# Optimization experiments

Hardware: AMD Instinct MI355X
Metric: run time of the kernel (lower is better)

Reference implementation:

```python
import jax, jax.numpy as jnp
import numpy as np

B, CIN, T, H, W = 1, 256, 64, 32, 32
A, G = 8, 8
SCALES = jnp.array([1., 2., 4., 8., 16., 32., 64., 128.], dtype=jnp.float32)
FEAT_STRIDE = 8.0
NMS_TOP_N = 100
NMS_THRESH = 0.7
MIN_SIZE = 4.0
POS_THR, NEG_THR = 0.7, 0.3
NEG_INF = -1e9


def _conv3d(x, w, b, strides):
    y = jax.lax.conv_general_dilated(
        x, w, window_strides=strides, padding=[(1, 1)] * 3,
        dimension_numbers=('NCDHW', 'OIDHW', 'NCDHW'))
    return y + b[None, :, None, None, None]


def _iou(a, b):
    # 1D interval IoU; a, b broadcastable [..., 2] = (start, end)
    inter = jnp.maximum(jnp.minimum(a[..., 1], b[..., 1]) - jnp.maximum(a[..., 0], b[..., 0]), 0.0)
    union = (a[..., 1] - a[..., 0]) + (b[..., 1] - b[..., 0]) - inter
    return inter / jnp.maximum(union, 1e-6)


def _nms(boxes, scores):
    # greedy 1D NMS: boxes [N,2], scores [N] -> top NMS_TOP_N (zero-padded)
    n = scores.shape[0]
    def step(sc, _):
        i = jnp.argmax(sc)
        s, box = sc[i], boxes[i]
        sup = (_iou(box[None], boxes) > NMS_THRESH) | (jnp.arange(n) == i)
        return jnp.where(sup, NEG_INF, sc), (box, s)
    _, (kb, ks) = jax.lax.scan(step, scores, None, length=NMS_TOP_N)
    keep = ks > NEG_INF * 0.5
    return jnp.where(keep[:, None], kb, 0.0), jnp.where(keep, ks, 0.0)


def _forward(base_feat, gt_chunks, video_len, c1w, c1b, c2w, c2b, sw, sb, dw, db):
    bsz = base_feat.shape[0]
    x = _conv3d(base_feat, c1w, c1b, (1, 2, 2))
    x = _conv3d(x, c2w, c2b, (1, 2, 2))
    feat = jnp.max(x, axis=(3, 4))                       # AdaptiveMaxPool3d((None,1,1)) -> [B,512,T]
    tlen = feat.shape[2]
    score_logit = (jnp.einsum('oc,bct->bot', sw, feat) + sb[None, :, None]).reshape(bsz, 2, A, tlen)
    delta = (jnp.einsum('oc,bct->bot', dw, feat) + db[None, :, None]).reshape(bsz, 2, A, tlen)
    prob = jax.nn.softmax(score_logit, axis=1)
    logp = jax.nn.log_softmax(score_logit, axis=1)

    # anchors: A lengths x T temporal positions, flattened as a*T + t
    anchor_len = FEAT_STRIDE * SCALES                                    # [A]
    centers = (jnp.arange(tlen, dtype=jnp.float32) + 0.5) * FEAT_STRIDE  # [T]
    a_start = centers[None, :] - anchor_len[:, None] / 2                 # [A,T]
    a_end = centers[None, :] + anchor_len[:, None] / 2
    anchors = jnp.stack([a_start, a_end], -1).reshape(-1, 2)             # [N,2]
    N = A * tlen

    # ---- proposal decode + NMS ----
    dc, dl = delta[:, 0], delta[:, 1]                                    # [B,A,T]
    pc = centers[None, None, :] + dc * anchor_len[None, :, None]
    pl = anchor_len[None, :, None] * jnp.exp(jnp.clip(dl, -10.0, 10.0))
    lim = tlen * FEAT_STRIDE
    ps = jnp.clip(pc - pl / 2, 0.0, lim)
    pe = jnp.clip(pc + pl / 2, 0.0, lim)
    boxes = jnp.stack([ps, pe], -1).reshape(bsz, N, 2)
    fg = prob[:, 1].reshape(bsz, N)
    fg = jnp.where((pe - ps).reshape(bsz, N) >= MIN_SIZE, fg, NEG_INF)
    prop_coord, prop_score = jax.vmap(_nms)(boxes, fg)

    # ---- IoU-based label assignment ----
    ious = _iou(anchors[None, :, None, :], gt_chunks[:, None, :, :])     # [B,N,G]
    max_iou = ious.max(-1)
    arg = ious.argmax(-1)                                                # [B,N]
    label = jnp.where(max_iou < NEG_THR, 0, -1)
    label = jnp.where(max_iou >= POS_THR, 1, label)
    best = ious.argmax(1)                                                # best anchor per gt [B,G]
    bidx = jnp.arange(bsz)[:, None]
    label = label.at[bidx, best].set(1)
    vl = video_len.astype(jnp.float32)[:, None]
    inside = (anchors[None, :, 0] >= 0.0) & (anchors[None, :, 1] <= vl)
    label = jnp.where(inside, label, -1)

    matched = gt_chunks[bidx, arg]                                       # [B,N,2]
    gc = (matched[..., 0] + matched[..., 1]) / 2
    gl = jnp.maximum(matched[..., 1] - matched[..., 0], 1e-6)
    ac = (anchors[:, 0] + anchors[:, 1]) / 2
    al = anchors[:, 1] - anchors[:, 0]
    reg_label = jnp.stack([(gc - ac[None]) / al[None], jnp.log(gl / al[None])], -1)
    reg_label = jax.lax.stop_gradient(reg_label)                          # targets carry no grad

    # ---- losses ----
    logp2 = logp.reshape(bsz, 2, N).transpose(0, 2, 1)                   # [B,N,2]
    lab = jnp.maximum(label, 0)
    nll = -jnp.take_along_axis(logp2, lab[..., None], axis=2)[..., 0]
    mask = (label >= 0).astype(jnp.float32)
    cls_loss = (nll * mask).sum() / jnp.maximum(mask.sum(), 1.0)

    delta2 = delta.reshape(bsz, 2, N).transpose(0, 2, 1)                 # [B,N,2]
    d = delta2 - reg_label
    sl1 = jnp.where(jnp.abs(d) < 1.0, 0.5 * d * d, jnp.abs(d) - 0.5).sum(-1)
    pos = (label == 1).astype(jnp.float32)
    reg_loss = (sl1 * pos).sum() / jnp.maximum(pos.sum(), 1.0)
    return prop_coord, prop_score, cls_loss, reg_loss


def setup_inputs() -> dict:
    key = jax.random.key(0)
    ks = jax.random.split(key, 8)
    base_feat = jax.random.normal(ks[0], (B, CIN, T, H, W), jnp.float32)
    starts = jax.random.uniform(ks[1], (B, G), minval=0.0, maxval=448.0)
    lens = jax.random.uniform(ks[2], (B, G), minval=8.0, maxval=64.0)
    gt_chunks = jnp.stack([starts, jnp.clip(starts + lens, 0.0, T * FEAT_STRIDE)], -1)
    video_len = jnp.full((B,), int(T * FEAT_STRIDE), jnp.int32)
    s = 0.02
    return dict(
        base_feat=base_feat, gt_chunks=gt_chunks, video_len=video_len,
        conv1_w=jax.random.normal(ks[3], (512, CIN, 3, 3, 3), jnp.float32) * s,
        conv1_b=jnp.zeros((512,), jnp.float32),
        conv2_w=jax.random.normal(ks[4], (512, 512, 3, 3, 3), jnp.float32) * s,
        conv2_b=jnp.zeros((512,), jnp.float32),
        score_w=jax.random.normal(ks[5], (2 * A, 512), jnp.float32) * s,
        score_b=jnp.zeros((2 * A,), jnp.float32),
        delta_w=jax.random.normal(ks[6], (2 * A, 512), jnp.float32) * s,
        delta_b=jnp.zeros((2 * A,), jnp.float32),
    )


def reference(base_feat, gt_chunks, video_len, conv1_w, conv1_b, conv2_w, conv2_b, score_w, score_b, delta_w, delta_b):
    return _forward(base_feat, gt_chunks, video_len, conv1_w, conv1_b, conv2_w, conv2_b, score_w, score_b, delta_w, delta_b)
```

## Files before the change

### kernel.cpp

```cpp
#include <hip/hip_runtime.h>

typedef __attribute__((ext_vector_type(8))) _Float16 half8;
typedef __attribute__((ext_vector_type(4))) _Float16 half4;
typedef __attribute__((ext_vector_type(4))) float floatx4;

#define DI __device__ __forceinline__

DI void gl_lds16(const void* g, void* l) {
    __builtin_amdgcn_global_load_lds(
        (__attribute__((address_space(1))) void*)(g),
        (__attribute__((address_space(3))) void*)(l), 16, 0, 0);
}


__global__ __launch_bounds__(256) void wt_split_t(
        const float* __restrict__ w1, _Float16* __restrict__ w1I,
        const float* __restrict__ w2, _Float16* __restrict__ w2I,
        float* __restrict__ zp) {
    __shared__ float L[13824];
    const int b = blockIdx.x;
    const int tid = threadIdx.x;
    if (b == 0 && tid < 64) zp[tid] = 0.0f;
    if (b < 512) {
        const float* src = w1 + (size_t)b * 6912;
        for (int idx = tid; idx < 6912; idx += 256) L[idx] = src[idx] * 64.0f;
        __syncthreads();
        for (int c = tid; c < 864; c += 256) {
            const int tap = c >> 5, o = c & 31;
            half8 h, l;
#pragma unroll
            for (int j = 0; j < 8; ++j) {
                const float x = L[(o * 8 + j) * 27 + tap];
                const _Float16 hh = (_Float16)x;
                h[j] = hh; l[j] = (_Float16)(x - (float)hh);
            }
            const size_t off = (size_t)b * 13824 + (size_t)(tap * 8 + (o >> 2)) * 64 + (o & 3) * 8;
            *(half8*)&w1I[off] = h;
            *(half8*)&w1I[off + 32] = l;
        }
    } else {
        const float* src = w2 + (size_t)(b - 512) * 13824;
        for (int idx = tid; idx < 13824; idx += 256) L[idx] = src[idx] * 64.0f;
        __syncthreads();
        for (int c = tid; c < 1728; c += 256) {
            const int tap = c >> 6, o = c & 63;
            half8 h, l;
#pragma unroll
            for (int j = 0; j < 8; ++j) {
                const float x = L[(o * 8 + j) * 27 + tap];
                const _Float16 hh = (_Float16)x;
                h[j] = hh; l[j] = (_Float16)(x - (float)hh);
            }
            const size_t off = (size_t)(b - 512) * 27648 + (size_t)(tap * 16 + (o >> 2)) * 64 + (o & 3) * 8;
            *(half8*)&w2I[off] = h;
            *(half8*)&w2I[off + 32] = l;
        }
    }
}

__global__ __launch_bounds__(256) void in_split(const float* __restrict__ in,
                                                _Float16* __restrict__ oI) {
    __shared__ float T[128 * 65];
    const int hb = blockIdx.x;
    const int s0 = blockIdx.y * 64;
    const int tid = threadIdx.x;
    const int cil = tid >> 1, part = tid & 1;
    const float* src = in + (size_t)(hb * 128 + cil) * 65536 + s0 + part * 32;
    float v[32];
#pragma unroll
    for (int q = 0; q < 8; ++q) *(float4*)(v + q * 4) = *(const float4*)(src + q * 4);
#pragma unroll
    for (int j = 0; j < 32; ++j) T[cil * 65 + part * 32 + j] = v[j];
    __syncthreads();
#pragma unroll
    for (int k = 0; k < 4; ++k) {
        const int c = tid + k * 256;
        const int sp = c >> 4, ol = c & 15;
        half8 h, l;
#pragma unroll
        for (int j = 0; j < 8; ++j) {
            const float x = T[(ol * 8 + j) * 65 + sp];
            const _Float16 hh = (_Float16)x;
            h[j] = hh; l[j] = (_Float16)(x - (float)hh);
        }
        const int og = hb * 16 + ol;
        const size_t off = (size_t)(s0 + sp) * 512 + (size_t)(og >> 2) * 64 + (og & 3) * 8;
        *(half8*)&oI[off] = h;
        *(half8*)&oI[off + 32] = l;
    }
}

__global__ __launch_bounds__(256, 2) void conv1_mfma(
        const _Float16* __restrict__ xI, const _Float16* __restrict__ wI,
        const float* __restrict__ b1, const _Float16* __restrict__ zp,
        _Float16* __restrict__ yI) {
    __shared__ __align__(16) _Float16 A2[2][128 * 64];
    __shared__ __align__(16) _Float16 B2[2][128 * 64];
    const int tid = threadIdx.x;
    const int co_blk = blockIdx.x;
    const int t = blockIdx.y;
    const int h0 = blockIdx.z * 8;
    const int wid = tid >> 6, lane = tid & 63;
    const int wm = wid & 1, wn = wid >> 1;
    const int ml = lane & 15, ql = lane >> 4;
    const int cs0 = (ql ^ (ml & 7)) * 8;
    const int cs1 = ((4 + ql) ^ (ml & 7)) * 8;
    const int sl = lane & 7, rl = lane >> 3;
    const int lc = sl ^ rl;

    const _Float16* wA[4]; const _Float16* bB[4];
    int dstq[4]; bool hok[4], wok[4];
    const size_t wbo = (size_t)co_blk * 128 * 13824;
#pragma unroll
    for (int q = 0; q < 4; ++q) {
        const int row = (q * 4 + wid) * 8 + rl;
        wA[q] = wI + wbo + (size_t)row * 13824 + lc * 8;
        dstq[q] = (q * 4 + wid) * 512 + lane * 8;
        const int h = h0 + (row >> 4), w = row & 15;
        const int ih2 = 2 * h - 1, iw2 = 2 * w - 1;
        hok[q] = (ih2 >= 0); wok[q] = (iw2 >= 0);
        bB[q] = xI + (ptrdiff_t)(ih2 * 32 + iw2) * 512 + lc * 8;
    }
    const _Float16* zpl = zp + lc * 8;

    floatx4 zz = {0.f, 0.f, 0.f, 0.f};
    floatx4 acc[4][4];
#pragma unroll
    for (int i = 0; i < 4; ++i)
#pragma unroll
        for (int j = 0; j < 4; ++j) acc[i][j] = zz;

    auto stage = [&](int kt, int cb, int KH, int KW, _Float16* Ad, _Float16* Bd) {
        const int it = t + kt - 1;
        const bool tok = ((unsigned)it < 64u);
        const size_t ab = (size_t)(((kt * 9 + KH * 3 + KW) * 8 + cb) * 64);
        const ptrdiff_t boff = (ptrdiff_t)it * 524288 + KH * 16384 + KW * 512 + cb * 64;
#pragma unroll
        for (int q = 0; q < 4; ++q) {
            gl_lds16(wA[q] + ab, &Ad[dstq[q]]);
            const bool ok = tok && (KH > 0 || hok[q]) && (KW > 0 || wok[q]);
            const _Float16* s = ok ? (bB[q] + boff) : zpl;
            gl_lds16(s, &Bd[dstq[q]]);
        }
    };

    stage(0, 0, 0, 0, A2[0], B2[0]);
    for (int o = 0; o < 24; ++o) {
        const int cb = o / 3, kt = o - cb * 3;
#pragma unroll
        for (int j = 0; j < 9; ++j) {
            __syncthreads();
            const int par = (o + j) & 1;
            if (j < 8) {
                stage(kt, cb, (j + 1) / 3, (j + 1) % 3, A2[par ^ 1], B2[par ^ 1]);
            } else if (o < 23) {
                stage((o + 1) % 3, (o + 1) / 3, 0, 0, A2[par ^ 1], B2[par ^ 1]);
            }
            const _Float16* Ab = A2[par];
            const _Float16* Bb = B2[par];
            half8 ah[4], alo[4], bh8[4], blo[4];
#pragma unroll
            for (int mi = 0; mi < 4; ++mi) {
                ah[mi]  = *(const half8*)&Ab[(wm * 64 + mi * 16 + ml) * 64 + cs0];
                alo[mi] = *(const half8*)&Ab[(wm * 64 + mi * 16 + ml) * 64 + cs1];
            }
#pragma unroll
            for (int ni = 0; ni < 4; ++ni) {
                bh8[ni] = *(const half8*)&Bb[(wn * 64 + ni * 16 + ml) * 64 + cs0];
                blo[ni] = *(const half8*)&Bb[(wn * 64 + ni * 16 + ml) * 64 + cs1];
            }
            __builtin_amdgcn_s_setprio(1);
#pragma unroll
            for (int mi = 0; mi < 4; ++mi)
#pragma unroll
                for (int ni = 0; ni < 4; ++ni) {
                    acc[mi][ni] = __builtin_amdgcn_mfma_f32_16x16x32_f16(ah[mi],  bh8[ni], acc[mi][ni], 0, 0, 0);
                    acc[mi][ni] = __builtin_amdgcn_mfma_f32_16x16x32_f16(ah[mi],  blo[ni], acc[mi][ni], 0, 0, 0);
                    acc[mi][ni] = __builtin_amdgcn_mfma_f32_16x16x32_f16(alo[mi], bh8[ni], acc[mi][ni], 0, 0, 0);
                }
            __builtin_amdgcn_s_setprio(0);
        }
    }

    const int qr = ql * 4;
#pragma unroll
    for (int mi = 0; mi < 4; ++mi) {
        const int co = co_blk * 128 + wm * 64 + mi * 16 + qr;
#pragma unroll
        for (int ni = 0; ni < 4; ++ni) {
            const int n = wn * 64 + ni * 16 + ml;
            const int h = h0 + (n >> 4), w = n & 15;
            const size_t base = ((size_t)t * 256 + h * 16 + w) * 1024
                              + (size_t)(co >> 5) * 64 + (co & 31);
            half4 hv, lv;
#pragma unroll
            for (int r = 0; r < 4; ++r) {
                const float v = acc[mi][ni][r] * 0.015625f + b1[co + r];
                const _Float16 hb = (_Float16)v;
                hv[r] = hb;
                lv[r] = (_Float16)(v - (float)hb);
            }
            *(half4*)(yI + base) = hv;
            *(half4*)(yI + base + 32) = lv;
        }
    }
}

__global__ __launch_bounds__(256, 2) void conv2_mfma(
        const _Float16* __restrict__ xI, const _Float16* __restrict__ wI,
        const _Float16* __restrict__ zp,
        float* __restrict__ x2p) {
    __shared__ __align__(16) _Float16 A2[2][128 * 64];
    __shared__ __align__(16) _Float16 B2[2][128 * 64];
    const int tid = threadIdx.x;
    const int co_blk = blockIdx.x;
    const int tp = blockIdx.y;
    const int ks = blockIdx.z;
    const int wid = tid >> 6, lane = tid & 63;
    const int wm = wid & 1, wn = wid >> 1;
    const int ml = lane & 15, ql = lane >> 4;
    const int cs0 = (ql ^ (ml & 7)) * 8;
    const int cs1 = ((4 + ql) ^ (ml & 7)) * 8;
    const int sl = lane & 7, rl = lane >> 3;
    const int lc = sl ^ rl;

    const _Float16* wA[4]; const _Float16* bB[4];
    int dstq[4], itv[4]; bool hok[4], wok[4];
    const size_t wbo = (size_t)co_blk * 128 * 27648;
#pragma unroll
    for (int q = 0; q < 4; ++q) {
        const int row = (q * 4 + wid) * 8 + rl;
        wA[q] = wI + wbo + (size_t)row * 27648 + lc * 8;
        dstq[q] = (q * 4 + wid) * 512 + lane * 8;
        const int sp = row & 63;
        itv[q] = tp * 2 + (row >> 6) - 1;
        const int ih2 = 2 * (sp >> 3) - 1, iw2 = 2 * (sp & 7) - 1;
        hok[q] = (ih2 >= 0); wok[q] = (iw2 >= 0);
        bB[q] = xI + (ptrdiff_t)((itv[q] * 256 + ih2 * 16 + iw2) * 1024) + lc * 8;
    }
    const _Float16* zpl = zp + lc * 8;

    floatx4 zz = {0.f, 0.f, 0.f, 0.f};
    floatx4 acc[4][4];
#pragma unroll
    for (int i = 0; i < 4; ++i)
#pragma unroll
        for (int j = 0; j < 4; ++j) acc[i][j] = zz;

    auto stage = [&](int kt, int cb, int KH, int KW, _Float16* Ad, _Float16* Bd) {
        const size_t ab = (size_t)(((kt * 9 + KH * 3 + KW) * 16 + cb) * 64);
        const ptrdiff_t boff = (ptrdiff_t)kt * 262144 + KH * 16384 + KW * 1024 + cb * 64;
#pragma unroll
        for (int q = 0; q < 4; ++q) {
            gl_lds16(wA[q] + ab, &Ad[dstq[q]]);
            const bool ok = ((unsigned)(itv[q] + kt) < 64u)
                         && (KH > 0 || hok[q]) && (KW > 0 || wok[q]);
            const _Float16* s = ok ? (bB[q] + boff) : zpl;
            gl_lds16(s, &Bd[dstq[q]]);
        }
    };

    stage(0, ks * 4, 0, 0, A2[0], B2[0]);
    for (int o = 0; o < 12; ++o) {
        const int kt = o % 3, cb = ks * 4 + o / 3;
#pragma unroll
        for (int j = 0; j < 9; ++j) {
            __syncthreads();
            const int par = (o + j) & 1;
            if (j < 8) {
                stage(kt, cb, (j + 1) / 3, (j + 1) % 3, A2[par ^ 1], B2[par ^ 1]);
            } else if (o < 11) {
                stage((o + 1) % 3, ks * 4 + (o + 1) / 3, 0, 0, A2[par ^ 1], B2[par ^ 1]);
            }
            const _Float16* Ab = A2[par];
            const _Float16* Bb = B2[par];
            half8 ah[4], alo[4], bh8[4], blo[4];
#pragma unroll
            for (int mi = 0; mi < 4; ++mi) {
                ah[mi]  = *(const half8*)&Ab[(wm * 64 + mi * 16 + ml) * 64 + cs0];
                alo[mi] = *(const half8*)&Ab[(wm * 64 + mi * 16 + ml) * 64 + cs1];
            }
#pragma unroll
            for (int ni = 0; ni < 4; ++ni) {
                bh8[ni] = *(const half8*)&Bb[(wn * 64 + ni * 16 + ml) * 64 + cs0];
                blo[ni] = *(const half8*)&Bb[(wn * 64 + ni * 16 + ml) * 64 + cs1];
            }
            __builtin_amdgcn_s_setprio(1);
#pragma unroll
            for (int mi = 0; mi < 4; ++mi)
#pragma unroll
                for (int ni = 0; ni < 4; ++ni) {
                    acc[mi][ni] = __builtin_amdgcn_mfma_f32_16x16x32_f16(ah[mi],  bh8[ni], acc[mi][ni], 0, 0, 0);
                    acc[mi][ni] = __builtin_amdgcn_mfma_f32_16x16x32_f16(ah[mi],  blo[ni], acc[mi][ni], 0, 0, 0);
                    acc[mi][ni] = __builtin_amdgcn_mfma_f32_16x16x32_f16(alo[mi], bh8[ni], acc[mi][ni], 0, 0, 0);
                }
            __builtin_amdgcn_s_setprio(0);
        }
    }

    const int qr = ql * 4;
#pragma unroll
    for (int mi = 0; mi < 4; ++mi) {
        const int co = co_blk * 128 + wm * 64 + mi * 16 + qr;
#pragma unroll
        for (int ni = 0; ni < 4; ++ni) {
            const int n = wn * 64 + ni * 16 + ml;
            const int ng = tp * 128 + n;
            float4 v;
            v.x = acc[mi][ni][0]; v.y = acc[mi][ni][1];
            v.z = acc[mi][ni][2]; v.w = acc[mi][ni][3];
            *(float4*)&x2p[((size_t)ks * 4096 + ng) * 512 + co] = v;
        }
    }
}

__global__ __launch_bounds__(256) void feat_head(
        const float* __restrict__ x2p, const float* __restrict__ b2,
        const float* __restrict__ sw, const float* __restrict__ sb,
        const float* __restrict__ dw, const float* __restrict__ db,
        float* __restrict__ scoreL, float* __restrict__ deltaL) {
    __shared__ float fr[512];
    __shared__ float partial[32][8];
    const int t = blockIdx.x, tid = threadIdx.x;
#pragma unroll
    for (int cc = 0; cc < 2; ++cc) {
        const int c = tid + cc * 256;
        float mx = -3.4e38f;
        for (int sp = 0; sp < 64; ++sp) {
            const size_t ng = (size_t)t * 64 + sp;
            const float s = x2p[ng * 512 + c]
                          + x2p[((size_t)4096 + ng) * 512 + c]
                          + x2p[((size_t)8192 + ng) * 512 + c]
                          + x2p[((size_t)12288 + ng) * 512 + c];
            mx = fmaxf(mx, s);
        }
        fr[c] = mx * 0.015625f + b2[c];
    }
    __syncthreads();
    const int o = tid & 31, part = tid >> 5;
    const float* wrow = (o < 16) ? (sw + (size_t)o * 512) : (dw + (size_t)(o - 16) * 512);
    float s = 0.f;
    const int j0 = part * 64;
#pragma unroll 16
    for (int j = 0; j < 64; ++j) s += wrow[j0 + j] * fr[j0 + j];
    partial[o][part] = s;
    __syncthreads();
    if (tid < 32) {
        float tot = 0.f;
#pragma unroll
        for (int p = 0; p < 8; ++p) tot += partial[tid][p];
        tot += (tid < 16) ? sb[tid] : db[tid - 16];
        if (tid < 16) scoreL[tid * 64 + t] = tot;
        else deltaL[(tid - 16) * 64 + t] = tot;
    }
}

__global__ void nms_loss_kernel(const float* __restrict__ scoreL,
                                const float* __restrict__ deltaL,
                                const float* __restrict__ gt,
                                const int* __restrict__ video_len,
                                float* __restrict__ out) {
    const int lane = threadIdx.x & 63;
    float gsv[8], gev[8];
#pragma unroll
    for (int g = 0; g < 8; ++g) { gsv[g] = gt[2 * g]; gev[g] = gt[2 * g + 1]; }
    const float center = ((float)lane + 0.5f) * 8.0f;
    float psv[8], pev[8], fg[8], l0v[8], l1v[8], dcv[8], dlv[8];
#pragma unroll
    for (int j = 0; j < 8; ++j) {
        const float s0 = scoreL[j * 64 + lane], s1 = scoreL[(8 + j) * 64 + lane];
        const float mm = fmaxf(s0, s1);
        const float lse = mm + logf(expf(s0 - mm) + expf(s1 - mm));
        l0v[j] = s0 - lse; l1v[j] = s1 - lse;
        const float dc = deltaL[j * 64 + lane], dl = deltaL[(8 + j) * 64 + lane];
        dcv[j] = dc; dlv[j] = dl;
        const float alen = 8.0f * (float)(1 << j);
        const float pc = center + dc * alen;
        const float pl = alen * expf(fminf(fmaxf(dl, -10.0f), 10.0f));
        const float ps = fminf(fmaxf(pc - pl * 0.5f, 0.0f), 512.0f);
        const float pe = fminf(fmaxf(pc + pl * 0.5f, 0.0f), 512.0f);
        psv[j] = ps; pev[j] = pe;
        fg[j] = ((pe - ps) >= 4.0f) ? expf(l1v[j]) : -1e9f;
    }
    for (int itn = 0; itn < 100; ++itn) {
        float v = fg[0]; int idx = lane;
#pragma unroll
        for (int j = 1; j < 8; ++j) if (fg[j] > v) { v = fg[j]; idx = lane + 64 * j; }
#pragma unroll
        for (int off = 32; off > 0; off >>= 1) {
            const float ov = __shfl_down(v, off);
            const int oi = __shfl_down(idx, off);
            if (ov > v || (ov == v && oi < idx)) { v = ov; idx = oi; }
        }
        v = __shfl(v, 0); idx = __shfl(idx, 0);
        const int wj = idx >> 6, wl = idx & 63;
        float bw0 = 0.f, bw1 = 0.f;
#pragma unroll
        for (int j = 0; j < 8; ++j) if (j == wj) { bw0 = psv[j]; bw1 = pev[j]; }
        const float b0 = __shfl(bw0, wl);
        const float b1 = __shfl(bw1, wl);
        if (lane == 0) {
            const bool kept = v > -5e8f;
            out[2 * itn] = kept ? b0 : 0.0f;
            out[2 * itn + 1] = kept ? b1 : 0.0f;
            out[200 + itn] = kept ? v : 0.0f;
        }
#pragma unroll
        for (int j = 0; j < 8; ++j) {
            const int n = lane + 64 * j;
            const float inter = fmaxf(fminf(b1, pev[j]) - fmaxf(b0, psv[j]), 0.0f);
            const float uni = (b1 - b0) + (pev[j] - psv[j]) - inter;
            const float iou = inter / fmaxf(uni, 1e-6f);
            if (iou > 0.7f || n == idx) fg[j] = -1e9f;
        }
    }
    int labv[8], aggv[8];
#pragma unroll
    for (int j = 0; j < 8; ++j) {
        const float alen = 8.0f * (float)(1 << j);
        const float as_ = center - alen * 0.5f, ae_ = center + alen * 0.5f;
        float mx = -1.0f; int ag = 0;
#pragma unroll
        for (int g = 0; g < 8; ++g) {
            const float inter = fmaxf(fminf(ae_, gev[g]) - fmaxf(as_, gsv[g]), 0.0f);
            const float uni = (ae_ - as_) + (gev[g] - gsv[g]) - inter;
            const float iou = inter / fmaxf(uni, 1e-6f);
            if (iou > mx) { mx = iou; ag = g; }
        }
        labv[j] = (mx < 0.3f) ? 0 : ((mx >= 0.7f) ? 1 : -1);
        aggv[j] = ag;
    }
    for (int g = 0; g < 8; ++g) {
        float v = -1.0f; int idx = 0;
#pragma unroll
        for (int j = 0; j < 8; ++j) {
            const int n = lane + 64 * j;
            const float alen = 8.0f * (float)(1 << j);
            const float as_ = center - alen * 0.5f, ae_ = center + alen * 0.5f;
            const float inter = fmaxf(fminf(ae_, gev[g]) - fmaxf(as_, gsv[g]), 0.0f);
            const float uni = (ae_ - as_) + (gev[g] - gsv[g]) - inter;
            const float iou = inter / fmaxf(uni, 1e-6f);
            if (iou > v || (iou == v && n < idx)) { v = iou; idx = n; }
        }
#pragma unroll
        for (int off = 32; off > 0; off >>= 1) {
            const float ov = __shfl_down(v, off);
            const int oi = __shfl_down(idx, off);
            if (ov > v || (ov == v && oi < idx)) { v = ov; idx = oi; }
        }
        idx = __shfl(idx, 0);
#pragma unroll
        for (int j = 0; j < 8; ++j)
            if (lane == (idx & 63) && j == (idx >> 6)) labv[j] = 1;
    }
    const float vl = (float)video_len[0];
    float nll_s = 0.f, msk_s = 0.f, reg_s = 0.f, pos_s = 0.f;
#pragma unroll
    for (int j = 0; j < 8; ++j) {
        const float alen = 8.0f * (float)(1 << j);
        const float as_ = center - alen * 0.5f, ae_ = center + alen * 0.5f;
        int l = labv[j];
        if (!((as_ >= 0.0f) && (ae_ <= vl))) l = -1;
        if (l >= 0) {
            msk_s += 1.0f;
            nll_s -= (l == 1) ? l1v[j] : l0v[j];
            if (l == 1) {
                pos_s += 1.0f;
                float gcv = 0.f, glv = 0.f;
#pragma unroll
                for (int g = 0; g < 8; ++g)
                    if (g == aggv[j]) {
                        gcv = (gsv[g] + gev[g]) * 0.5f;
                        glv = fmaxf(gev[g] - gsv[g], 1e-6f);
                    }
                const float r0 = (gcv - center) / alen;
                const float r1 = logf(glv / alen);
                const float d0 = dcv[j] - r0, d1 = dlv[j] - r1;
                float s = (fabsf(d0) < 1.0f) ? (0.5f * d0 * d0) : (fabsf(d0) - 0.5f);
                s += (fabsf(d1) < 1.0f) ? (0.5f * d1 * d1) : (fabsf(d1) - 0.5f);
                reg_s += s;
            }
        }
    }
    float sums[4] = {nll_s, msk_s, reg_s, pos_s};
#pragma unroll
    for (int k = 0; k < 4; ++k)
#pragma unroll
        for (int off = 32; off > 0; off >>= 1) sums[k] += __shfl_down(sums[k], off);
    if (lane == 0) {
        out[300] = sums[0] / fmaxf(sums[1], 1.0f);
        out[301] = sums[2] / fmaxf(sums[3], 1.0f);
    }
}

extern "C" void kernel_launch(void* const* d_in, const int* in_sizes, int n_in,
                              void* d_out, int out_size, void* d_ws, size_t ws_size,
                              hipStream_t stream) {
    const float* base_feat = (const float*)d_in[0];
    const float* gt        = (const float*)d_in[1];
    const int*   video_len = (const int*)d_in[2];
    const float* w1        = (const float*)d_in[3];
    const float* b1        = (const float*)d_in[4];
    const float* w2        = (const float*)d_in[5];
    const float* b2        = (const float*)d_in[6];
    const float* sw        = (const float*)d_in[7];
    const float* sb        = (const float*)d_in[8];
    const float* dw        = (const float*)d_in[9];
    const float* db        = (const float*)d_in[10];

    char* ws = (char*)d_ws;
    _Float16* w1I = (_Float16*)ws;  ws += (size_t)512 * 13824 * 2;
    _Float16* w2I = (_Float16*)ws;  ws += (size_t)512 * 27648 * 2;
    _Float16* inI = (_Float16*)ws;  ws += (size_t)65536 * 512 * 2;
    _Float16* x1I = (_Float16*)ws;  ws += (size_t)16384 * 1024 * 2;
    float* scoreL = (float*)ws;     ws += (size_t)16 * 64 * 4;
    float* deltaL = (float*)ws;     ws += (size_t)16 * 64 * 4;
    float* zpage  = (float*)ws;     ws += (size_t)64 * 4;
    float* x2p = (float*)inI;

    wt_split_t<<<1024, 256, 0, stream>>>(w1, w1I, w2, w2I, zpage);
    in_split<<<dim3(2, 1024), 256, 0, stream>>>(base_feat, inI);
    conv1_mfma<<<dim3(4, 64, 2), 256, 0, stream>>>(inI, w1I, b1,
                                                   (const _Float16*)zpage, x1I);
    conv2_mfma<<<dim3(4, 32, 4), 256, 0, stream>>>(x1I, w2I,
                                                   (const _Float16*)zpage, x2p);
    feat_head<<<64, 256, 0, stream>>>(x2p, b2, sw, sb, dw, db, scoreL, deltaL);
    nms_loss_kernel<<<1, 64, 0, stream>>>(scoreL, deltaL, gt, video_len,
                                          (float*)d_out);
}
```

Before: 747.8 us.

## Triple-buffer activation tiles with prefetch distance two in conv MFMA kernels

Splits staging into separate weight and activation loaders in both conv kernels. Weights stay double-buffered in LDS, while activations move to a three-slot ring that is prefetched two steps ahead. The per-step __syncthreads is replaced by an explicit s_waitcnt vmcnt(4) plus barrier at the end of each step, so the newest activation loads can stay in flight across the barrier and global latency is hidden more deeply. In exchange, LDS per block grows from 64 KB to 80 KB, which is tight for two blocks per CU, and the final step issues harmless extra prefetches past the reduction range.

```diff
diff --git a/kernel.cpp b/kernel.cpp
--- a/kernel.cpp
+++ b/kernel.cpp
@@ -95,7 +95,7 @@
         const float* __restrict__ b1, const _Float16* __restrict__ zp,
         _Float16* __restrict__ yI) {
     __shared__ __align__(16) _Float16 A2[2][128 * 64];
-    __shared__ __align__(16) _Float16 B2[2][128 * 64];
+    __shared__ __align__(16) _Float16 B3[3][128 * 64];
     const int tid = threadIdx.x;
     const int co_blk = blockIdx.x;
     const int t = blockIdx.y;
@@ -130,34 +130,43 @@
 #pragma unroll
         for (int j = 0; j < 4; ++j) acc[i][j] = zz;
 
-    auto stage = [&](int kt, int cb, int KH, int KW, _Float16* Ad, _Float16* Bd) {
+    auto stageA = [&](int kt, int cb, int KH, int KW, _Float16* Ad) {
+        const size_t ab = (size_t)(((kt * 9 + KH * 3 + KW) * 8 + cb) * 64);
+#pragma unroll
+        for (int q = 0; q < 4; ++q) gl_lds16(wA[q] + ab, &Ad[dstq[q]]);
+    };
+    auto stageB = [&](int kt, int cb, int KH, int KW, _Float16* Bd) {
         const int it = t + kt - 1;
         const bool tok = ((unsigned)it < 64u);
-        const size_t ab = (size_t)(((kt * 9 + KH * 3 + KW) * 8 + cb) * 64);
         const ptrdiff_t boff = (ptrdiff_t)it * 524288 + KH * 16384 + KW * 512 + cb * 64;
 #pragma unroll
         for (int q = 0; q < 4; ++q) {
-            gl_lds16(wA[q] + ab, &Ad[dstq[q]]);
             const bool ok = tok && (KH > 0 || hok[q]) && (KW > 0 || wok[q]);
-            const _Float16* s = ok ? (bB[q] + boff) : zpl;
-            gl_lds16(s, &Bd[dstq[q]]);
+            gl_lds16(ok ? (bB[q] + boff) : zpl, &Bd[dstq[q]]);
         }
     };
 
-    stage(0, 0, 0, 0, A2[0], B2[0]);
+    stageA(0, 0, 0, 0, A2[0]);
+    stageB(0, 0, 0, 0, B3[0]);
+    stageB(0, 0, 0, 1, B3[1]);
+    asm volatile("s_waitcnt vmcnt(4)" ::: "memory");
+    __builtin_amdgcn_s_barrier();
+
     for (int o = 0; o < 24; ++o) {
         const int cb = o / 3, kt = o - cb * 3;
+        const int o1 = o + 1;
+        const int cb1 = o1 / 3, kt1 = o1 - cb1 * 3;
 #pragma unroll
         for (int j = 0; j < 9; ++j) {
-            __syncthreads();
             const int par = (o + j) & 1;
-            if (j < 8) {
-                stage(kt, cb, (j + 1) / 3, (j + 1) % 3, A2[par ^ 1], B2[par ^ 1]);
-            } else if (o < 23) {
-                stage((o + 1) % 3, (o + 1) / 3, 0, 0, A2[par ^ 1], B2[par ^ 1]);
-            }
+            if (j < 8) stageA(kt, cb, (j + 1) / 3, (j + 1) % 3, A2[par ^ 1]);
+            else       stageA(kt1, cb1, 0, 0, A2[par ^ 1]);
+            if (j < 7)       stageB(kt, cb, (j + 2) / 3, (j + 2) % 3, B3[(j + 2) % 3]);
+            else if (j == 7) stageB(kt1, cb1, 0, 0, B3[0]);
+            else             stageB(kt1, cb1, 0, 1, B3[1]);
+
             const _Float16* Ab = A2[par];
-            const _Float16* Bb = B2[par];
+            const _Float16* Bb = B3[j % 3];
             half8 ah[4], alo[4], bh8[4], blo[4];
 #pragma unroll
             for (int mi = 0; mi < 4; ++mi) {
@@ -179,6 +188,8 @@
                     acc[mi][ni] = __builtin_amdgcn_mfma_f32_16x16x32_f16(alo[mi], bh8[ni], acc[mi][ni], 0, 0, 0);
                 }
             __builtin_amdgcn_s_setprio(0);
+            asm volatile("s_waitcnt vmcnt(4)" ::: "memory");
+            __builtin_amdgcn_s_barrier();
         }
     }
 
@@ -211,7 +222,7 @@
         const _Float16* __restrict__ zp,
         float* __restrict__ x2p) {
     __shared__ __align__(16) _Float16 A2[2][128 * 64];
-    __shared__ __align__(16) _Float16 B2[2][128 * 64];
+    __shared__ __align__(16) _Float16 B3[3][128 * 64];
     const int tid = threadIdx.x;
     const int co_blk = blockIdx.x;
     const int tp = blockIdx.y;
@@ -247,33 +258,42 @@
 #pragma unroll
         for (int j = 0; j < 4; ++j) acc[i][j] = zz;
 
-    auto stage = [&](int kt, int cb, int KH, int KW, _Float16* Ad, _Float16* Bd) {
+    auto stageA = [&](int kt, int cb, int KH, int KW, _Float16* Ad) {
         const size_t ab = (size_t)(((kt * 9 + KH * 3 + KW) * 16 + cb) * 64);
+#pragma unroll
+        for (int q = 0; q < 4; ++q) gl_lds16(wA[q] + ab, &Ad[dstq[q]]);
+    };
+    auto stageB = [&](int kt, int cb, int KH, int KW, _Float16* Bd) {
         const ptrdiff_t boff = (ptrdiff_t)kt * 262144 + KH * 16384 + KW * 1024 + cb * 64;
 #pragma unroll
         for (int q = 0; q < 4; ++q) {
-            gl_lds16(wA[q] + ab, &Ad[dstq[q]]);
             const bool ok = ((unsigned)(itv[q] + kt) < 64u)
                          && (KH > 0 || hok[q]) && (KW > 0 || wok[q]);
-            const _Float16* s = ok ? (bB[q] + boff) : zpl;
-            gl_lds16(s, &Bd[dstq[q]]);
+            gl_lds16(ok ? (bB[q] + boff) : zpl, &Bd[dstq[q]]);
         }
     };
 
-    stage(0, ks * 4, 0, 0, A2[0], B2[0]);
+    stageA(0, ks * 4, 0, 0, A2[0]);
+    stageB(0, ks * 4, 0, 0, B3[0]);
+    stageB(0, ks * 4, 0, 1, B3[1]);
+    asm volatile("s_waitcnt vmcnt(4)" ::: "memory");
+    __builtin_amdgcn_s_barrier();
+
     for (int o = 0; o < 12; ++o) {
         const int kt = o % 3, cb = ks * 4 + o / 3;
+        const int o1 = o + 1;
+        const int kt1 = o1 % 3, cb1 = ks * 4 + o1 / 3;
 #pragma unroll
         for (int j = 0; j < 9; ++j) {
-            __syncthreads();
             const int par = (o + j) & 1;
-            if (j < 8) {
-                stage(kt, cb, (j + 1) / 3, (j + 1) % 3, A2[par ^ 1], B2[par ^ 1]);
-            } else if (o < 11) {
-                stage((o + 1) % 3, ks * 4 + (o + 1) / 3, 0, 0, A2[par ^ 1], B2[par ^ 1]);
-            }
+            if (j < 8) stageA(kt, cb, (j + 1) / 3, (j + 1) % 3, A2[par ^ 1]);
+            else       stageA(kt1, cb1, 0, 0, A2[par ^ 1]);
+            if (j < 7)       stageB(kt, cb, (j + 2) / 3, (j + 2) % 3, B3[(j + 2) % 3]);
+            else if (j == 7) stageB(kt1, cb1, 0, 0, B3[0]);
+            else             stageB(kt1, cb1, 0, 1, B3[1]);
+
             const _Float16* Ab = A2[par];
-            const _Float16* Bb = B2[par];
+            const _Float16* Bb = B3[j % 3];
             half8 ah[4], alo[4], bh8[4], blo[4];
 #pragma unroll
             for (int mi = 0; mi < 4; ++mi) {
@@ -295,6 +315,8 @@
                     acc[mi][ni] = __builtin_amdgcn_mfma_f32_16x16x32_f16(alo[mi], bh8[ni], acc[mi][ni], 0, 0, 0);
                 }
             __builtin_amdgcn_s_setprio(0);
+            asm volatile("s_waitcnt vmcnt(4)" ::: "memory");
+            __builtin_amdgcn_s_barrier();
         }
     }
 
```

New measurement: 756.2 us. Within noise of the previous version (+1.1%).
